# Optimization experiments

Hardware: AMD Instinct MI355X
Metric: run time of the kernel (lower is better)

The kernel has to match this reference:

```python
import jax, jax.numpy as jnp
import numpy as np

B, L, H, Z, T = 128, 4096, 1024, 256, 16  # batch, input_len(64*64), lstm_hidden, z_size, timesteps


def _lstm_cell(x, h, c, W_ih, b_ih, W_hh, b_hh):
    # PyTorch LSTMCell: gates ordered (input, forget, cell, output)
    gates = x @ W_ih.T + b_ih + h @ W_hh.T + b_hh
    i, f, g, o = jnp.split(gates, 4, axis=-1)
    c_new = jax.nn.sigmoid(f) * c + jax.nn.sigmoid(i) * jnp.tanh(g)
    h_new = jax.nn.sigmoid(o) * jnp.tanh(c_new)
    return h_new, c_new


def setup_inputs() -> dict:
    key = jax.random.key(0)
    ks = jax.random.split(key, 16)
    s = 0.02  # weight init scale
    return {
        "x": jax.random.uniform(ks[0], (B, L), dtype=jnp.float32),
        "eps": jax.random.normal(ks[1], (T, B, Z), dtype=jnp.float32),
        "c_0": jax.random.normal(ks[2], (1, L), dtype=jnp.float32),
        "h_0_enc": jax.random.normal(ks[3], (H,), dtype=jnp.float32),
        "h_0_dec": jax.random.normal(ks[4], (H,), dtype=jnp.float32),
        "W_ih_enc": jax.random.normal(ks[5], (4 * H, 2 * L + H), dtype=jnp.float32) * s,
        "b_ih_enc": jnp.zeros((4 * H,), dtype=jnp.float32),
        "W_hh_enc": jax.random.normal(ks[6], (4 * H, H), dtype=jnp.float32) * s,
        "b_hh_enc": jnp.zeros((4 * H,), dtype=jnp.float32),
        "W_mu": jax.random.normal(ks[7], (Z, H), dtype=jnp.float32) * s,
        "b_mu": jnp.zeros((Z,), dtype=jnp.float32),
        "W_sigma": jax.random.normal(ks[8], (Z, H), dtype=jnp.float32) * s,
        "b_sigma": jnp.zeros((Z,), dtype=jnp.float32),
        "W_ih_dec": jax.random.normal(ks[9], (4 * H, Z), dtype=jnp.float32) * s,
        "b_ih_dec": jnp.zeros((4 * H,), dtype=jnp.float32),
        "W_hh_dec": jax.random.normal(ks[10], (4 * H, H), dtype=jnp.float32) * s,
        "b_hh_dec": jnp.zeros((4 * H,), dtype=jnp.float32),
        "W_write": jax.random.normal(ks[11], (L, H), dtype=jnp.float32) * s,
        "b_write": jnp.zeros((L,), dtype=jnp.float32),
    }


def reference(x, eps, c_0, h_0_enc, h_0_dec,
              W_ih_enc, b_ih_enc, W_hh_enc, b_hh_enc,
              W_mu, b_mu, W_sigma, b_sigma,
              W_ih_dec, b_ih_dec, W_hh_dec, b_hh_dec,
              W_write, b_write):
    batch = x.shape[0]
    c_t = jnp.broadcast_to(c_0, (batch, L))
    h_enc = jnp.broadcast_to(h_0_enc, (batch, H))
    h_dec = jnp.broadcast_to(h_0_dec, (batch, H))
    c_enc = jnp.zeros((batch, H), dtype=x.dtype)
    c_dec = jnp.zeros((batch, H), dtype=x.dtype)

    def step(carry, eps_t):
        c_t, h_enc, c_enc, h_dec, c_dec = carry
        x_hat = x - jax.nn.sigmoid(c_t)
        r_t = jnp.concatenate((x, x_hat, h_dec), axis=-1)  # read + concat with h_dec
        h_enc, c_enc = _lstm_cell(r_t, h_enc, c_enc, W_ih_enc, b_ih_enc, W_hh_enc, b_hh_enc)
        mu = h_enc @ W_mu.T + b_mu
        logsigma = h_enc @ W_sigma.T + b_sigma
        z_t = eps_t * jnp.exp(logsigma) + mu
        h_dec, c_dec = _lstm_cell(z_t, h_dec, c_dec, W_ih_dec, b_ih_dec, W_hh_dec, b_hh_dec)
        c_t = c_t + h_dec @ W_write.T + b_write
        return (c_t, h_enc, c_enc, h_dec, c_dec), None

    (c_t, _, _, _, _), _ = jax.lax.scan(step, (c_t, h_enc, c_enc, h_dec, c_dec), eps)
    return jax.nn.sigmoid(c_t)
```

## Files before the change

### kernel.cpp

```cpp
#include <hip/hip_runtime.h>

#define B_   128
#define T_   16

typedef __bf16 bf16;
typedef __bf16 bf16x4 __attribute__((ext_vector_type(4)));
typedef __bf16 bf16x8 __attribute__((ext_vector_type(8)));
typedef float f32x4 __attribute__((ext_vector_type(4)));

#define GLL(SRC, DST) __builtin_amdgcn_global_load_lds( \
    (const __attribute__((address_space(1))) void*)(SRC), \
    (__attribute__((address_space(3))) void*)(DST), 16, 0, 0)

#define MFMA __builtin_amdgcn_mfma_f32_16x16x32_bf16
#define SLICE 524288

__device__ __forceinline__ float sigf(float x) { return 1.f / (1.f + expf(-x)); }

__device__ __forceinline__ void core64(
    bf16 (&As)[2][4096], bf16 (&Bs)[2][4096],
    const bf16* __restrict__ Ab, int lda,
    const bf16* __restrict__ Wb, int ldw,
    int nk, f32x4 (&acc)[4])
{
    const int tid = threadIdx.x, lane = tid & 63, wave = tid >> 6;
    const int srow = lane >> 3;
    const int scol = ((lane & 7) ^ srow) << 3;
    const int wr = wave & 1, wc = wave >> 1;
    const int ln = lane & 15;
    const int rA0 = wr * 32 + ln;
    const int rB0 = wc * 32 + ln;
    const int swz = (lane & 7) << 4;
    const int kq  = (lane >> 4) << 4;

    auto stage = [&](int b, int koff) {
        int c0 = wave, c1 = wave + 4;
        int ra0 = c0 * 8 + srow, ra1 = c1 * 8 + srow;
        GLL(Ab + (size_t)ra0 * lda + koff + scol, &As[b][c0 * 512]);
        GLL(Ab + (size_t)ra1 * lda + koff + scol, &As[b][c1 * 512]);
        GLL(Wb + (size_t)ra0 * ldw + koff + scol, &Bs[b][c0 * 512]);
        GLL(Wb + (size_t)ra1 * ldw + koff + scol, &Bs[b][c1 * 512]);
    };

    stage(0, 0);
    int bq = 0;
    for (int it = 0; it < nk; ++it) {
        __syncthreads();
        if (it + 1 < nk) stage(bq ^ 1, (it + 1) << 6);
        const bf16* as = As[bq];
        const bf16* bs = Bs[bq];
#pragma unroll
        for (int k2 = 0; k2 < 2; ++k2) {
            const int co = (((k2 << 6) | kq) ^ swz) >> 1;
            bf16x8 a0 = *(const bf16x8*)&as[rA0 * 64 + co];
            bf16x8 a1 = *(const bf16x8*)&as[(rA0 + 16) * 64 + co];
            bf16x8 b0 = *(const bf16x8*)&bs[rB0 * 64 + co];
            bf16x8 b1 = *(const bf16x8*)&bs[(rB0 + 16) * 64 + co];
            acc[0] = MFMA(a0, b0, acc[0], 0, 0, 0);
            acc[1] = MFMA(a0, b1, acc[1], 0, 0, 0);
            acc[2] = MFMA(a1, b0, acc[2], 0, 0, 0);
            acc[3] = MFMA(a1, b1, acc[3], 0, 0, 0);
        }
        bq ^= 1;
    }
}

__device__ __forceinline__ void store64f(float* __restrict__ P, int bm, int bn,
                                         f32x4 (&acc)[4])
{
    const int lane = threadIdx.x & 63, wave = threadIdx.x >> 6;
    const int wr = wave & 1, wc = wave >> 1;
    const int ln = lane & 15, q = lane >> 4;
    const int row0 = bm + wr * 32 + q * 4;
    const int col0 = bn + wc * 32 + ln;
#pragma unroll
    for (int r = 0; r < 4; ++r) {
        P[(size_t)(row0 + r) * 4096 + col0]           = acc[0][r];
        P[(size_t)(row0 + r) * 4096 + col0 + 16]      = acc[1][r];
        P[(size_t)(row0 + 16 + r) * 4096 + col0]      = acc[2][r];
        P[(size_t)(row0 + 16 + r) * 4096 + col0 + 16] = acc[3][r];
    }
}

__device__ __forceinline__ void store64b(bf16* __restrict__ P, int bm, int bn,
                                         f32x4 (&acc)[4])
{
    const int lane = threadIdx.x & 63, wave = threadIdx.x >> 6;
    const int wr = wave & 1, wc = wave >> 1;
    const int ln = lane & 15, q = lane >> 4;
    const int row0 = bm + wr * 32 + q * 4;
    const int col0 = bn + wc * 32 + ln;
#pragma unroll
    for (int r = 0; r < 4; ++r) {
        P[(size_t)(row0 + r) * 4096 + col0]           = (bf16)acc[0][r];
        P[(size_t)(row0 + r) * 4096 + col0 + 16]      = (bf16)acc[1][r];
        P[(size_t)(row0 + 16 + r) * 4096 + col0]      = (bf16)acc[2][r];
        P[(size_t)(row0 + 16 + r) * 4096 + col0 + 16] = (bf16)acc[3][r];
    }
}

__global__ __launch_bounds__(256) void gemm64_k(
    const bf16* __restrict__ A, int lda,
    const bf16* __restrict__ W, int ldw, int Kc,
    float* __restrict__ P)
{
    __shared__ bf16 As[2][4096], Bs[2][4096];
    const int nt = blockIdx.x, mt = blockIdx.y, zz = blockIdx.z;
    f32x4 acc[4];
#pragma unroll
    for (int i = 0; i < 4; ++i) acc[i] = (f32x4){0.f, 0.f, 0.f, 0.f};
    const bf16* Ab = A + (size_t)mt * 64 * lda + (size_t)zz * Kc;
    const bf16* Wb = W + (size_t)nt * 64 * ldw + (size_t)zz * Kc;
    core64(As, Bs, Ab, lda, Wb, ldw, Kc >> 6, acc);
    store64f(P + (size_t)zz * SLICE, mt * 64, nt * 64, acc);
}

__global__ __launch_bounds__(256) void gemm64b_k(
    const bf16* __restrict__ A, int lda,
    const bf16* __restrict__ W, int ldw, int Kc,
    bf16* __restrict__ P)
{
    __shared__ bf16 As[2][4096], Bs[2][4096];
    const int nt = blockIdx.x, mt = blockIdx.y, zz = blockIdx.z;
    f32x4 acc[4];
#pragma unroll
    for (int i = 0; i < 4; ++i) acc[i] = (f32x4){0.f, 0.f, 0.f, 0.f};
    const bf16* Ab = A + (size_t)mt * 64 * lda + (size_t)zz * Kc;
    const bf16* Wb = W + (size_t)nt * 64 * ldw + (size_t)zz * Kc;
    core64(As, Bs, Ab, lda, Wb, ldw, Kc >> 6, acc);
    store64b(P + (size_t)zz * SLICE, mt * 64, nt * 64, acc);
}

__global__ __launch_bounds__(256) void kE_k(
    const bf16* __restrict__ hh,   const bf16* __restrict__ Wwr,
    const bf16* __restrict__ Wcat, const bf16* __restrict__ Wdh,
    bf16* __restrict__ wrP, bf16* __restrict__ encP, bf16* __restrict__ decP,
    int zoff)
{
    __shared__ bf16 As[2][4096], Bs[2][4096];
    const int nt = blockIdx.x, mt = blockIdx.y, zz = blockIdx.z + zoff;
    f32x4 acc[4];
#pragma unroll
    for (int i = 0; i < 4; ++i) acc[i] = (f32x4){0.f, 0.f, 0.f, 0.f};

    const bf16* Ab;
    const bf16* Wb;
    int ldw;
    bf16* P;
    if (zz < 2) {
        Ab = hh + (size_t)mt * 64 * 2048 + zz * 512;
        Wb = Wwr + (size_t)nt * 64 * 1024 + zz * 512;
        ldw = 1024; P = wrP + (size_t)zz * SLICE;
    } else if (zz < 6) {
        int s = zz - 2;
        Ab = hh + (size_t)mt * 64 * 2048 + s * 512;
        Wb = Wcat + (size_t)nt * 64 * 2048 + s * 512;
        ldw = 2048; P = encP + (size_t)(8 + s) * SLICE;
    } else {
        int g = zz - 6;
        Ab = hh + (size_t)mt * 64 * 2048 + g * 512;
        Wb = Wdh + (size_t)nt * 64 * 1024 + g * 512;
        ldw = 1024; P = decP + (size_t)g * SLICE;
    }
    core64(As, Bs, Ab, 2048, Wb, ldw, 8, acc);
    store64b(P, mt * 64, nt * 64, acc);
}

__global__ __launch_bounds__(256) void fin0_k(
    const float* __restrict__ P, float* __restrict__ base,
    const float* __restrict__ b1, const float* __restrict__ b2)
{
    const int i = blockIdx.x * 256 + threadIdx.x;
    const int row = i >> 10, j = i & 1023;
    const size_t off = (size_t)row * 4096 + (j << 2);
    float s0 = 0.f, s1 = 0.f, s2 = 0.f, s3 = 0.f;
#pragma unroll
    for (int z = 0; z < 4; ++z) {
        float4 p = *(const float4*)(P + (size_t)z * SLICE + off);
        s0 += p.x; s1 += p.y; s2 += p.z; s3 += p.w;
    }
    base[off + 0] = s0 + b1[j]        + b2[j];
    base[off + 1] = s1 + b1[1024 + j] + b2[1024 + j];
    base[off + 2] = s2 + b1[2048 + j] + b2[2048 + j];
    base[off + 3] = s3 + b1[3072 + j] + b2[3072 + j];
}

__global__ __launch_bounds__(256) void kB_k(
    const bf16* __restrict__ encP, const float* __restrict__ base,
    float* __restrict__ c_enc, bf16* __restrict__ hh)
{
    const int i = blockIdx.x * 256 + threadIdx.x;
    const int row = i >> 10, j = i & 1023;
    const size_t off = (size_t)row * 4096 + (j << 2);
    float s0 = 0.f, s1 = 0.f, s2 = 0.f, s3 = 0.f;
#pragma unroll
    for (int z = 0; z < 12; ++z) {
        bf16x4 p = *(const bf16x4*)(encP + (size_t)z * SLICE + off);
        s0 += (float)p[0]; s1 += (float)p[1]; s2 += (float)p[2]; s3 += (float)p[3];
    }
    float4 bb = *(const float4*)(base + off);
    float gi = s0 + bb.x, gf = s1 + bb.y, gg = s2 + bb.z, go = s3 + bb.w;
    float cn = sigf(gf) * c_enc[i] + sigf(gi) * tanhf(gg);
    c_enc[i] = cn;
    hh[(size_t)row * 2048 + 1024 + j] = (bf16)(sigf(go) * tanhf(cn));
}

__global__ __launch_bounds__(256) void kF_k(
    const bf16* __restrict__ wrP, const float* __restrict__ b_wr,
    float* __restrict__ c_t, bf16* __restrict__ negs, float* __restrict__ outp)
{
    const int qi = blockIdx.x * 256 + threadIdx.x;
    const int row = qi >> 10, cq = qi & 1023;
    const size_t off = (size_t)row * 4096 + (cq << 2);
    bf16x4 p0 = *(const bf16x4*)(wrP + off);
    bf16x4 p1 = *(const bf16x4*)(wrP + SLICE + off);
    float4 cv = *(const float4*)(c_t + off);
    float4 bw = *(const float4*)(b_wr + (cq << 2));
    float v0 = cv.x + (float)p0[0] + (float)p1[0] + bw.x;
    float v1 = cv.y + (float)p0[1] + (float)p1[1] + bw.y;
    float v2 = cv.z + (float)p0[2] + (float)p1[2] + bw.z;
    float v3 = cv.w + (float)p0[3] + (float)p1[3] + bw.w;
    *(float4*)(c_t + off) = make_float4(v0, v1, v2, v3);
    negs[off + 0] = (bf16)(-sigf(v0));
    negs[off + 1] = (bf16)(-sigf(v1));
    negs[off + 2] = (bf16)(-sigf(v2));
    negs[off + 3] = (bf16)(-sigf(v3));
    if (outp)
        *(float4*)(outp + off) = make_float4(sigf(v0), sigf(v1), sigf(v2), sigf(v3));
}

struct SmemG32 {
    bf16 As[4][128][64];
    bf16 Ws[4][32][64];
};

__global__ __launch_bounds__(256) void kC_k(
    const bf16* __restrict__ hh, const bf16* __restrict__ Wms,
    const float* __restrict__ b_mu, const float* __restrict__ b_sig,
    const float* __restrict__ eps_t, bf16* __restrict__ zbf)
{
    __shared__ SmemG32 sm;
    const int nt = blockIdx.x;
    const int tid = threadIdx.x, lane = tid & 63, wave = tid >> 6;
    const int srow = lane >> 3, scol = ((lane & 7) ^ srow) << 3;
    const int ln = lane & 15, kq = (lane >> 4) << 4;
    const int swz = (lane & 7) << 4;
    const int rA = wave * 32 + ln;
    const bf16* Wb = Wms + (size_t)nt * 32 * 1024;
    const bf16* Ab = hh + 1024;

    f32x4 acc[2][2];
#pragma unroll
    for (int m = 0; m < 2; ++m)
#pragma unroll
        for (int n = 0; n < 2; ++n) acc[m][n] = (f32x4){0.f, 0.f, 0.f, 0.f};

    for (int it = 0; it < 4; ++it) {
        if (it) __syncthreads();
        const int koff = it * 256;
#pragma unroll
        for (int kc = 0; kc < 4; ++kc) {
            const int kg = koff + kc * 64 + scol;
#pragma unroll
            for (int i = 0; i < 4; ++i) {
                int rb = i * 32 + wave * 8;
                GLL(Ab + (size_t)(rb + srow) * 2048 + kg, &sm.As[kc][rb][0]);
            }
            GLL(Wb + (size_t)(wave * 8 + srow) * 1024 + kg, &sm.Ws[kc][wave * 8][0]);
        }
        __syncthreads();
#pragma unroll
        for (int kc = 0; kc < 4; ++kc)
#pragma unroll
            for (int k2 = 0; k2 < 2; ++k2) {
                const int co = (((k2 << 6) | kq) ^ swz) >> 1;
                bf16x8 a0 = *(const bf16x8*)&sm.As[kc][rA][co];
                bf16x8 a1 = *(const bf16x8*)&sm.As[kc][rA + 16][co];
                bf16x8 b0 = *(const bf16x8*)&sm.Ws[kc][ln][co];
                bf16x8 b1 = *(const bf16x8*)&sm.Ws[kc][ln + 16][co];
                acc[0][0] = MFMA(a0, b0, acc[0][0], 0, 0, 0);
                acc[0][1] = MFMA(a0, b1, acc[0][1], 0, 0, 0);
                acc[1][0] = MFMA(a1, b0, acc[1][0], 0, 0, 0);
                acc[1][1] = MFMA(a1, b1, acc[1][1], 0, 0, 0);
            }
    }
    __syncthreads();

    float* Cl = (float*)&sm;
    const int q = lane >> 4;
#pragma unroll
    for (int f = 0; f < 2; ++f)
#pragma unroll
        for (int n = 0; n < 2; ++n)
#pragma unroll
            for (int r = 0; r < 4; ++r)
                Cl[(wave * 32 + f * 16 + q * 4 + r) * 33 + n * 16 + ln] = acc[f][n][r];
    __syncthreads();

#pragma unroll
    for (int it = 0; it < 8; ++it) {
        int li = it * 256 + tid;
        int row = li >> 4, zl = li & 15;
        int zi = nt * 16 + zl;
        float mu = Cl[row * 33 + zl * 2]     + b_mu[zi];
        float ls = Cl[row * 33 + zl * 2 + 1] + b_sig[zi];
        float z = eps_t[row * 256 + zi] * expf(ls) + mu;
        zbf[(size_t)row * 256 + zi] = (bf16)z;
    }
}

struct SmemD {
    bf16 As[4][128][64];
    bf16 Ws[4][64][64];
};

__global__ __launch_bounds__(256) void kD_k(
    const bf16* __restrict__ zbf, const bf16* __restrict__ Wdz,
    const bf16* __restrict__ decP,
    const float* __restrict__ b_ihd, const float* __restrict__ b_hhd,
    float* __restrict__ c_dec, bf16* __restrict__ hh)
{
    __shared__ SmemD sm;
    const int nt = blockIdx.x;
    const int tid = threadIdx.x, lane = tid & 63, wave = tid >> 6;
    const int srow = lane >> 3, scol = ((lane & 7) ^ srow) << 3;
    const int ln = lane & 15, q = lane >> 4;
    const int kq = q << 4, swz = (lane & 7) << 4;
    const int wr = wave & 1, wc = wave >> 1;
    const bf16* Wb = Wdz + (size_t)nt * 64 * 256;

    f32x4 acc[4][2];
#pragma unroll
    for (int f = 0; f < 4; ++f)
#pragma unroll
        for (int n = 0; n < 2; ++n) acc[f][n] = (f32x4){0.f, 0.f, 0.f, 0.f};

#pragma unroll
    for (int kc = 0; kc < 4; ++kc) {
        const int kg = kc * 64 + scol;
#pragma unroll
        for (int i = 0; i < 4; ++i) {
            int rb = i * 32 + wave * 8;
            GLL(zbf + (size_t)(rb + srow) * 256 + kg, &sm.As[kc][rb][0]);
        }
#pragma unroll
        for (int i = 0; i < 2; ++i) {
            int rbw = i * 32 + wave * 8;
            GLL(Wb + (size_t)(rbw + srow) * 256 + kg, &sm.Ws[kc][rbw][0]);
        }
    }
    __syncthreads();
#pragma unroll
    for (int kc = 0; kc < 4; ++kc)
#pragma unroll
        for (int k2 = 0; k2 < 2; ++k2) {
            const int co = (((k2 << 6) | kq) ^ swz) >> 1;
            bf16x8 b0 = *(const bf16x8*)&sm.Ws[kc][wc * 32 + ln][co];
            bf16x8 b1 = *(const bf16x8*)&sm.Ws[kc][wc * 32 + ln + 16][co];
#pragma unroll
            for (int f = 0; f < 4; ++f) {
                bf16x8 a = *(const bf16x8*)&sm.As[kc][wr * 64 + f * 16 + ln][co];
                acc[f][0] = MFMA(a, b0, acc[f][0], 0, 0, 0);
                acc[f][1] = MFMA(a, b1, acc[f][1], 0, 0, 0);
            }
        }
    __syncthreads();

    float* Cl = (float*)&sm;
#pragma unroll
    for (int f = 0; f < 4; ++f)
#pragma unroll
        for (int n = 0; n < 2; ++n)
#pragma unroll
            for (int r = 0; r < 4; ++r)
                Cl[(wr * 64 + f * 16 + q * 4 + r) * 66 + wc * 32 + n * 16 + ln] = acc[f][n][r];
    __syncthreads();

#pragma unroll
    for (int it = 0; it < 8; ++it) {
        int li = it * 256 + tid;
        int row = li >> 4, jl = li & 15;
        int J = nt * 16 + jl;
        const float* cr = &Cl[row * 66 + jl * 4];
        int gcol = nt * 64 + jl * 4;
        const bf16* gp = decP + (size_t)row * 4096 + gcol;
        bf16x4 g0v = *(const bf16x4*)gp;
        bf16x4 g1v = *(const bf16x4*)(gp + SLICE);
        float gi = cr[0] + (float)g0v[0] + (float)g1v[0] + b_ihd[J]        + b_hhd[J];
        float gf = cr[1] + (float)g0v[1] + (float)g1v[1] + b_ihd[1024 + J] + b_hhd[1024 + J];
        float gg = cr[2] + (float)g0v[2] + (float)g1v[2] + b_ihd[2048 + J] + b_hhd[2048 + J];
        float go = cr[3] + (float)g0v[3] + (float)g1v[3] + b_ihd[3072 + J] + b_hhd[3072 + J];
        int ci = row * 1024 + J;
        float cn = sigf(gf) * c_dec[ci] + sigf(gi) * tanhf(gg);
        c_dec[ci] = cn;
        hh[(size_t)row * 2048 + J] = (bf16)(sigf(go) * tanhf(cn));
    }
}

#define PBL (B_ * 4096)
#define PBH (B_ * 1024)

__global__ void init_k(const float* __restrict__ x, const float* __restrict__ c0,
                       const float* __restrict__ h0e, const float* __restrict__ h0d,
                       float* __restrict__ c_t, float* __restrict__ c_enc,
                       float* __restrict__ c_dec, bf16* __restrict__ negs,
                       bf16* __restrict__ hh, bf16* __restrict__ x_bf) {
    int i = blockIdx.x * 256 + threadIdx.x;
    if (i >= PBL) return;
    int n = i & 4095;
    float c = c0[n];
    c_t[i] = c;
    negs[i] = (bf16)(-sigf(c));
    x_bf[i] = (bf16)x[i];
    if (i < PBH) {
        int row = i >> 10, j = i & 1023;
        c_enc[i] = 0.f;
        c_dec[i] = 0.f;
        hh[(size_t)row * 2048 + j]        = (bf16)h0d[j];
        hh[(size_t)row * 2048 + 1024 + j] = (bf16)h0e[j];
    }
}

__device__ __forceinline__ bf16x8 cvt8(const float* s) {
    float4 a = *(const float4*)s, b = *(const float4*)(s + 4);
    bf16x8 v = { (bf16)a.x, (bf16)a.y, (bf16)a.z, (bf16)a.w,
                 (bf16)b.x, (bf16)b.y, (bf16)b.z, (bf16)b.w };
    return v;
}

__global__ void conv_es_k(const float* __restrict__ Wih, const float* __restrict__ Whh,
                          bf16* __restrict__ wxh, bf16* __restrict__ wsum,
                          bf16* __restrict__ wcat) {
    int id = blockIdx.x * 256 + threadIdx.x;
    if (id >= 4096 * 768) return;
    int np = id / 768, c = (id - np * 768) * 8;
    int n = ((np & 3) << 10) + (np >> 2);
    if (c < 4096) {
        const float* sx = Wih + (size_t)n * 9216 + c;
        const float* sh = sx + 4096;
        float4 a = *(const float4*)sh, b = *(const float4*)(sh + 4);
        float4 e = *(const float4*)sx, f = *(const float4*)(sx + 4);
        bf16x8 vh = { (bf16)a.x, (bf16)a.y, (bf16)a.z, (bf16)a.w,
                      (bf16)b.x, (bf16)b.y, (bf16)b.z, (bf16)b.w };
        bf16x8 vs = { (bf16)(a.x + e.x), (bf16)(a.y + e.y), (bf16)(a.z + e.z), (bf16)(a.w + e.w),
                      (bf16)(b.x + f.x), (bf16)(b.y + f.y), (bf16)(b.z + f.z), (bf16)(b.w + f.w) };
        *(bf16x8*)(wxh  + (size_t)np * 4096 + c) = vh;
        *(bf16x8*)(wsum + (size_t)np * 4096 + c) = vs;
    } else if (c < 5120) {
        *(bf16x8*)(wcat + (size_t)np * 2048 + (c - 4096)) =
            cvt8(Wih + (size_t)n * 9216 + 8192 + (c - 4096));
    } else {
        *(bf16x8*)(wcat + (size_t)np * 2048 + 1024 + (c - 5120)) =
            cvt8(Whh + (size_t)n * 1024 + (c - 5120));
    }
}

__global__ void conv_dec_k(const float* __restrict__ Wih, const float* __restrict__ Whh,
                           bf16* __restrict__ wdz, bf16* __restrict__ wdh) {
    int id = blockIdx.x * 256 + threadIdx.x;
    if (id >= 4096 * 160) return;
    int np = id / 160, c = (id - np * 160) * 8;
    int n = ((np & 3) << 10) + (np >> 2);
    if (c < 256)
        *(bf16x8*)(wdz + (size_t)np * 256 + c) = cvt8(Wih + (size_t)n * 256 + c);
    else
        *(bf16x8*)(wdh + (size_t)np * 1024 + (c - 256)) =
            cvt8(Whh + (size_t)n * 1024 + (c - 256));
}

__global__ void conv_ms_k(const float* __restrict__ Wmu, const float* __restrict__ Wsig,
                          bf16* __restrict__ dst) {
    int id = blockIdx.x * 256 + threadIdx.x;
    if (id >= 512 * 128) return;
    int np = id >> 7, c = (id & 127) * 8;
    int zi = np >> 1;
    const float* src = ((np & 1) ? Wsig : Wmu) + (size_t)zi * 1024 + c;
    *(bf16x8*)(dst + (size_t)np * 1024 + c) = cvt8(src);
}

__global__ void conv_wr_k(const float* __restrict__ Wwr, bf16* __restrict__ dst) {
    int id = blockIdx.x * 256 + threadIdx.x;
    if (id >= 4096 * 128) return;
    *(bf16x8*)(dst + (size_t)id * 8) = cvt8(Wwr + (size_t)id * 8);
}

extern "C" void kernel_launch(void* const* d_in, const int* in_sizes, int n_in,
                              void* d_out, int out_size, void* d_ws, size_t ws_size,
                              hipStream_t stream) {
    const float* x      = (const float*)d_in[0];
    const float* eps    = (const float*)d_in[1];
    const float* c0     = (const float*)d_in[2];
    const float* h0e    = (const float*)d_in[3];
    const float* h0d    = (const float*)d_in[4];
    const float* W_ih_e = (const float*)d_in[5];
    const float* b_ih_e = (const float*)d_in[6];
    const float* W_hh_e = (const float*)d_in[7];
    const float* b_hh_e = (const float*)d_in[8];
    const float* W_mu   = (const float*)d_in[9];
    const float* b_mu   = (const float*)d_in[10];
    const float* W_sig  = (const float*)d_in[11];
    const float* b_sig  = (const float*)d_in[12];
    const float* W_ih_d = (const float*)d_in[13];
    const float* b_ih_d = (const float*)d_in[14];
    const float* W_hh_d = (const float*)d_in[15];
    const float* b_hh_d = (const float*)d_in[16];
    const float* W_wr   = (const float*)d_in[17];
    const float* b_wr   = (const float*)d_in[18];
    float* out = (float*)d_out;

    float* f = (float*)d_ws;
    float* c_t   = f; f += SLICE;
    float* base  = f; f += SLICE;
    float* pP    = f; f += (size_t)4 * SLICE;
    float* c_enc = f; f += 131072;
    float* c_dec = f; f += 131072;
    bf16* bp    = (bf16*)f;
    bf16* encP  = bp; bp += (size_t)12 * SLICE;
    bf16* decP  = bp; bp += (size_t)2 * SLICE;
    bf16* wrP   = bp; bp += (size_t)2 * SLICE;
    bf16* negs  = bp; bp += (size_t)B_ * 4096;
    bf16* hh    = bp; bp += (size_t)B_ * 2048;
    bf16* zbf   = bp; bp += (size_t)B_ * 256;
    bf16* x_bf  = bp; bp += (size_t)B_ * 4096;
    bf16* Wxh   = bp; bp += (size_t)4096 * 4096;
    bf16* Wsum  = bp; bp += (size_t)4096 * 4096;
    bf16* Wcat  = bp; bp += (size_t)4096 * 2048;
    bf16* Wdz   = bp; bp += (size_t)4096 * 256;
    bf16* Wdh   = bp; bp += (size_t)4096 * 1024;
    bf16* Wms   = bp; bp += (size_t)512 * 1024;
    bf16* Wwr   = bp; bp += (size_t)4096 * 1024;

    dim3 blk(256);

    init_k<<<(PBL + 255) / 256, blk, 0, stream>>>(x, c0, h0e, h0d, c_t, c_enc, c_dec,
                                                  negs, hh, x_bf);
    conv_es_k<<<(4096 * 768 + 255) / 256, blk, 0, stream>>>(W_ih_e, W_hh_e,
                                                            Wxh, Wsum, Wcat);
    conv_dec_k<<<(4096 * 160 + 255) / 256, blk, 0, stream>>>(W_ih_d, W_hh_d, Wdz, Wdh);
    conv_ms_k<<<(512 * 128 + 255) / 256, blk, 0, stream>>>(W_mu, W_sig, Wms);
    conv_wr_k<<<(4096 * 128 + 255) / 256, blk, 0, stream>>>(W_wr, Wwr);

    gemm64_k<<<dim3(64, 2, 4), blk, 0, stream>>>(x_bf, 4096, Wsum, 4096, 1024, pP);
    fin0_k<<<dim3(512), blk, 0, stream>>>(pP, base, b_ih_e, b_hh_e);

    kE_k<<<dim3(64, 2, 6), blk, 0, stream>>>(hh, Wwr, Wcat, Wdh, wrP, encP, decP, 2);

    for (int t = 0; t < T_; ++t) {
        gemm64b_k<<<dim3(64, 2, 8), blk, 0, stream>>>(negs, 4096, Wxh, 4096, 512, encP);
        kB_k<<<dim3(512), blk, 0, stream>>>(encP, base, c_enc, hh);
        kC_k<<<dim3(16), blk, 0, stream>>>(hh, Wms, b_mu, b_sig,
                                           eps + (size_t)t * (B_ * 256), zbf);
        kD_k<<<dim3(64), blk, 0, stream>>>(zbf, Wdz, decP, b_ih_d, b_hh_d, c_dec, hh);
        kE_k<<<dim3(64, 2, 8), blk, 0, stream>>>(hh, Wwr, Wcat, Wdh, wrP, encP, decP, 0);
        kF_k<<<dim3(512), blk, 0, stream>>>(wrP, b_wr, c_t, negs,
                                            (t == T_ - 1) ? out : nullptr);
    }
}
```

Before: 840.6 us.

## Merge encoder x_hat GEMM with hidden-state GEMMs and split write GEMM out

```diff
diff --git a/kernel.cpp b/kernel.cpp
--- a/kernel.cpp
+++ b/kernel.cpp
@@ -115,55 +115,57 @@
     store64f(P + (size_t)zz * SLICE, mt * 64, nt * 64, acc);
 }
 
-__global__ __launch_bounds__(256) void gemm64b_k(
-    const bf16* __restrict__ A, int lda,
-    const bf16* __restrict__ W, int ldw, int Kc,
-    bf16* __restrict__ P)
+__global__ __launch_bounds__(256) void kAE_k(
+    const bf16* __restrict__ negs, const bf16* __restrict__ hh,
+    const bf16* __restrict__ Wxh,  const bf16* __restrict__ Wcat,
+    const bf16* __restrict__ Wdh,
+    bf16* __restrict__ encP, bf16* __restrict__ decP)
 {
     __shared__ bf16 As[2][4096], Bs[2][4096];
-    const int nt = blockIdx.x, mt = blockIdx.y, zz = blockIdx.z;
+    const int bid = blockIdx.x;
+    const int swz = (bid & 7) * 224 + (bid >> 3);
+    const int mt = swz & 1, nt = (swz >> 1) & 63, zz = swz >> 7;
+
+    const bf16 *Ab, *Wb;
+    int lda, ldw;
+    bf16* P;
+    if (zz < 8) {
+        Ab = negs + (size_t)mt * 64 * 4096 + zz * 512; lda = 4096;
+        Wb = Wxh  + (size_t)nt * 64 * 4096 + zz * 512; ldw = 4096;
+        P = encP + (size_t)zz * SLICE;
+    } else if (zz < 12) {
+        int s = zz - 8;
+        Ab = hh   + (size_t)mt * 64 * 2048 + s * 512;  lda = 2048;
+        Wb = Wcat + (size_t)nt * 64 * 2048 + s * 512;  ldw = 2048;
+        P = encP + (size_t)(8 + s) * SLICE;
+    } else {
+        int g = zz - 12;
+        Ab = hh  + (size_t)mt * 64 * 2048 + g * 512;   lda = 2048;
+        Wb = Wdh + (size_t)nt * 64 * 1024 + g * 512;   ldw = 1024;
+        P = decP + (size_t)g * SLICE;
+    }
     f32x4 acc[4];
 #pragma unroll
     for (int i = 0; i < 4; ++i) acc[i] = (f32x4){0.f, 0.f, 0.f, 0.f};
-    const bf16* Ab = A + (size_t)mt * 64 * lda + (size_t)zz * Kc;
-    const bf16* Wb = W + (size_t)nt * 64 * ldw + (size_t)zz * Kc;
-    core64(As, Bs, Ab, lda, Wb, ldw, Kc >> 6, acc);
-    store64b(P + (size_t)zz * SLICE, mt * 64, nt * 64, acc);
-}
-
-__global__ __launch_bounds__(256) void kE_k(
-    const bf16* __restrict__ hh,   const bf16* __restrict__ Wwr,
-    const bf16* __restrict__ Wcat, const bf16* __restrict__ Wdh,
-    bf16* __restrict__ wrP, bf16* __restrict__ encP, bf16* __restrict__ decP,
-    int zoff)
+    core64(As, Bs, Ab, lda, Wb, ldw, 8, acc);
+    store64b(P, mt * 64, nt * 64, acc);
+}
+
+__global__ __launch_bounds__(256) void kW_k(
+    const bf16* __restrict__ hh, const bf16* __restrict__ Wwr,
+    bf16* __restrict__ wrP)
 {
     __shared__ bf16 As[2][4096], Bs[2][4096];
-    const int nt = blockIdx.x, mt = blockIdx.y, zz = blockIdx.z + zoff;
+    const int bid = blockIdx.x;
+    const int swz = (bid & 7) * 32 + (bid >> 3);
+    const int mt = swz & 1, nt = (swz >> 1) & 63, zz = swz >> 7;
+    const bf16* Ab = hh  + (size_t)mt * 64 * 2048 + zz * 512;
+    const bf16* Wb = Wwr + (size_t)nt * 64 * 1024 + zz * 512;
     f32x4 acc[4];
 #pragma unroll
     for (int i = 0; i < 4; ++i) acc[i] = (f32x4){0.f, 0.f, 0.f, 0.f};
-
-    const bf16* Ab;
-    const bf16* Wb;
-    int ldw;
-    bf16* P;
-    if (zz < 2) {
-        Ab = hh + (size_t)mt * 64 * 2048 + zz * 512;
-        Wb = Wwr + (size_t)nt * 64 * 1024 + zz * 512;
-        ldw = 1024; P = wrP + (size_t)zz * SLICE;
-    } else if (zz < 6) {
-        int s = zz - 2;
-        Ab = hh + (size_t)mt * 64 * 2048 + s * 512;
-        Wb = Wcat + (size_t)nt * 64 * 2048 + s * 512;
-        ldw = 2048; P = encP + (size_t)(8 + s) * SLICE;
-    } else {
-        int g = zz - 6;
-        Ab = hh + (size_t)mt * 64 * 2048 + g * 512;
-        Wb = Wdh + (size_t)nt * 64 * 1024 + g * 512;
-        ldw = 1024; P = decP + (size_t)g * SLICE;
-    }
-    core64(As, Bs, Ab, 2048, Wb, ldw, 8, acc);
-    store64b(P, mt * 64, nt * 64, acc);
+    core64(As, Bs, Ab, 2048, Wb, 1024, 8, acc);
+    store64b(wrP + (size_t)zz * SLICE, mt * 64, nt * 64, acc);
 }
 
 __global__ __launch_bounds__(256) void fin0_k(
@@ -309,10 +311,7 @@
     }
 }
 
-struct SmemD {
-    bf16 As[4][128][64];
-    bf16 Ws[4][64][64];
-};
+struct SmemK { bf16 A[2][4096]; bf16 B[2][4096]; };
 
 __global__ __launch_bounds__(256) void kD_k(
     const bf16* __restrict__ zbf, const bf16* __restrict__ Wdz,
@@ -320,70 +319,42 @@
     const float* __restrict__ b_ihd, const float* __restrict__ b_hhd,
     float* __restrict__ c_dec, bf16* __restrict__ hh)
 {
-    __shared__ SmemD sm;
-    const int nt = blockIdx.x;
+    __shared__ SmemK sm;
+    const int bid = blockIdx.x;
+    const int mt = bid & 1, nt = bid >> 1;
     const int tid = threadIdx.x, lane = tid & 63, wave = tid >> 6;
-    const int srow = lane >> 3, scol = ((lane & 7) ^ srow) << 3;
+    const int wr = wave & 1, wc = wave >> 1;
     const int ln = lane & 15, q = lane >> 4;
-    const int kq = q << 4, swz = (lane & 7) << 4;
-    const int wr = wave & 1, wc = wave >> 1;
+
+    const bf16* Ab = zbf + (size_t)mt * 64 * 256;
     const bf16* Wb = Wdz + (size_t)nt * 64 * 256;
-
-    f32x4 acc[4][2];
-#pragma unroll
-    for (int f = 0; f < 4; ++f)
-#pragma unroll
-        for (int n = 0; n < 2; ++n) acc[f][n] = (f32x4){0.f, 0.f, 0.f, 0.f};
-
-#pragma unroll
-    for (int kc = 0; kc < 4; ++kc) {
-        const int kg = kc * 64 + scol;
-#pragma unroll
-        for (int i = 0; i < 4; ++i) {
-            int rb = i * 32 + wave * 8;
-            GLL(zbf + (size_t)(rb + srow) * 256 + kg, &sm.As[kc][rb][0]);
-        }
-#pragma unroll
-        for (int i = 0; i < 2; ++i) {
-            int rbw = i * 32 + wave * 8;
-            GLL(Wb + (size_t)(rbw + srow) * 256 + kg, &sm.Ws[kc][rbw][0]);
-        }
-    }
+    f32x4 acc[4];
+#pragma unroll
+    for (int i = 0; i < 4; ++i) acc[i] = (f32x4){0.f, 0.f, 0.f, 0.f};
+    core64(sm.A, sm.B, Ab, 256, Wb, 256, 4, acc);
+
     __syncthreads();
-#pragma unroll
-    for (int kc = 0; kc < 4; ++kc)
-#pragma unroll
-        for (int k2 = 0; k2 < 2; ++k2) {
-            const int co = (((k2 << 6) | kq) ^ swz) >> 1;
-            bf16x8 b0 = *(const bf16x8*)&sm.Ws[kc][wc * 32 + ln][co];
-            bf16x8 b1 = *(const bf16x8*)&sm.Ws[kc][wc * 32 + ln + 16][co];
-#pragma unroll
-            for (int f = 0; f < 4; ++f) {
-                bf16x8 a = *(const bf16x8*)&sm.As[kc][wr * 64 + f * 16 + ln][co];
-                acc[f][0] = MFMA(a, b0, acc[f][0], 0, 0, 0);
-                acc[f][1] = MFMA(a, b1, acc[f][1], 0, 0, 0);
-            }
-        }
+    float* Cl = (float*)&sm;
+    const int r0 = wr * 32 + q * 4;
+    const int c0 = wc * 32 + ln;
+#pragma unroll
+    for (int r = 0; r < 4; ++r) {
+        Cl[(r0 + r) * 66 + c0]           = acc[0][r];
+        Cl[(r0 + r) * 66 + c0 + 16]      = acc[1][r];
+        Cl[(r0 + 16 + r) * 66 + c0]      = acc[2][r];
+        Cl[(r0 + 16 + r) * 66 + c0 + 16] = acc[3][r];
+    }
     __syncthreads();
 
-    float* Cl = (float*)&sm;
-#pragma unroll
-    for (int f = 0; f < 4; ++f)
-#pragma unroll
-        for (int n = 0; n < 2; ++n)
-#pragma unroll
-            for (int r = 0; r < 4; ++r)
-                Cl[(wr * 64 + f * 16 + q * 4 + r) * 66 + wc * 32 + n * 16 + ln] = acc[f][n][r];
-    __syncthreads();
-
-#pragma unroll
-    for (int it = 0; it < 8; ++it) {
+#pragma unroll
+    for (int it = 0; it < 4; ++it) {
         int li = it * 256 + tid;
-        int row = li >> 4, jl = li & 15;
-        int J = nt * 16 + jl;
-        const float* cr = &Cl[row * 66 + jl * 4];
-        int gcol = nt * 64 + jl * 4;
-        const bf16* gp = decP + (size_t)row * 4096 + gcol;
+        int lrow = li >> 4, jl = li & 15;
+        int row = mt * 64 + lrow;
+        int np0 = nt * 64 + jl * 4;
+        int J = np0 >> 2;
+        const float* cr = &Cl[lrow * 66 + jl * 4];
+        const bf16* gp = decP + (size_t)row * 4096 + np0;
         bf16x4 g0v = *(const bf16x4*)gp;
         bf16x4 g1v = *(const bf16x4*)(gp + SLICE);
         float gi = cr[0] + (float)g0v[0] + (float)g1v[0] + b_ihd[J]        + b_hhd[J];
@@ -543,16 +514,17 @@
     gemm64_k<<<dim3(64, 2, 4), blk, 0, stream>>>(x_bf, 4096, Wsum, 4096, 1024, pP);
     fin0_k<<<dim3(512), blk, 0, stream>>>(pP, base, b_ih_e, b_hh_e);
 
-    kE_k<<<dim3(64, 2, 6), blk, 0, stream>>>(hh, Wwr, Wcat, Wdh, wrP, encP, decP, 2);
+    kAE_k<<<dim3(1792), blk, 0, stream>>>(negs, hh, Wxh, Wcat, Wdh, encP, decP);
 
     for (int t = 0; t < T_; ++t) {
-        gemm64b_k<<<dim3(64, 2, 8), blk, 0, stream>>>(negs, 4096, Wxh, 4096, 512, encP);
         kB_k<<<dim3(512), blk, 0, stream>>>(encP, base, c_enc, hh);
         kC_k<<<dim3(16), blk, 0, stream>>>(hh, Wms, b_mu, b_sig,
                                            eps + (size_t)t * (B_ * 256), zbf);
-        kD_k<<<dim3(64), blk, 0, stream>>>(zbf, Wdz, decP, b_ih_d, b_hh_d, c_dec, hh);
-        kE_k<<<dim3(64, 2, 8), blk, 0, stream>>>(hh, Wwr, Wcat, Wdh, wrP, encP, decP, 0);
+        kD_k<<<dim3(128), blk, 0, stream>>>(zbf, Wdz, decP, b_ih_d, b_hh_d, c_dec, hh);
+        kW_k<<<dim3(256), blk, 0, stream>>>(hh, Wwr, wrP);
         kF_k<<<dim3(512), blk, 0, stream>>>(wrP, b_wr, c_t, negs,
                                             (t == T_ - 1) ? out : nullptr);
-    }
-}
+        if (t < T_ - 1)
+            kAE_k<<<dim3(1792), blk, 0, stream>>>(negs, hh, Wxh, Wcat, Wdh, encP, decP);
+    }
+}
```

Result: slower. 863.0 us (+2.7%).
